# Optimization experiments

Measured on AMD Instinct MI355X. Metric: run time of the kernel, lower is better.

The kernel has to match this reference:

```python
import jax, jax.numpy as jnp
import numpy as np

EPS = 1e-6
NUM_HEADS = 16
ROPE_THETA = 100000.0


def _rope_tables(seq_len, head_dim, theta):
    inv_freq = 1.0 / (theta ** (np.arange(0, head_dim, 2, dtype=np.float32) / head_dim))
    t = np.arange(seq_len, dtype=np.float32)
    freqs = np.outer(t, inv_freq)                      # (S, head_dim//2)
    emb = np.concatenate([freqs, freqs], axis=-1)      # (S, head_dim)
    return jnp.asarray(np.cos(emb))[None], jnp.asarray(np.sin(emb))[None]  # (1,S,D)


def setup_inputs() -> dict:
    key = jax.random.key(0)
    ks = jax.random.split(key, 6)
    B, S, H = 2, 2048, 1024
    head_dim = H // NUM_HEADS
    cos, sin = _rope_tables(S, head_dim, ROPE_THETA)
    scale = 0.02
    return {
        "hidden_states": jax.random.normal(ks[0], (B, S, H), dtype=jnp.float32),
        "cos": cos, "sin": sin,
        "Wq": jax.random.normal(ks[1], (H, H), dtype=jnp.float32) * scale,
        "bq": jnp.zeros((H,), dtype=jnp.float32),
        "Wk": jax.random.normal(ks[2], (H, H), dtype=jnp.float32) * scale,
        "bk": jnp.zeros((H,), dtype=jnp.float32),
        "Wv": jax.random.normal(ks[3], (H, H), dtype=jnp.float32) * scale,
        "bv": jnp.zeros((H,), dtype=jnp.float32),
        "Wo": jax.random.normal(ks[4], (H, H), dtype=jnp.float32) * scale,
        "bo": jnp.zeros((H,), dtype=jnp.float32),
        "rms_weight": jnp.ones((H,), dtype=jnp.float32),
    }


def _rms_norm(x, w):
    var = jnp.mean(x * x, axis=-1, keepdims=True)
    return x * jax.lax.rsqrt(var + EPS) * w


def _rotate_half(x):
    x1, x2 = jnp.split(x, 2, axis=-1)
    return jnp.concatenate([-x2, x1], axis=-1)


def reference(hidden_states, cos, sin, Wq, bq, Wk, bk, Wv, bv, Wo, bo, rms_weight):
    B, S, H = hidden_states.shape
    D = H // NUM_HEADS
    q = hidden_states @ Wq.T + bq
    k = hidden_states @ Wk.T + bk
    v = hidden_states @ Wv.T + bv
    # RMSNorm over full hidden dim BEFORE head split (as in original)
    q = _rms_norm(q, rms_weight)
    k = _rms_norm(k, rms_weight)
    # (B,S,H) -> (B,heads,S,D)
    q = q.reshape(B, S, NUM_HEADS, D).transpose(0, 2, 1, 3)
    k = k.reshape(B, S, NUM_HEADS, D).transpose(0, 2, 1, 3)
    v = v.reshape(B, S, NUM_HEADS, D).transpose(0, 2, 1, 3)
    # RoPE: cos/sin (1,S,D) -> unsqueeze head dim
    c = cos[:, None, :, :]
    s = sin[:, None, :, :]
    q = q * c + _rotate_half(q) * s
    k = k * c + _rotate_half(k) * s
    # attention (faithful: boolean tril mask is ADDED as 0/1, not -inf)
    scale = D ** 0.5
    scores = jnp.einsum("bhqd,bhkd->bhqk", q, k) / scale
    mask = jnp.tril(jnp.ones((S, S), dtype=scores.dtype))  # +1 on causal, +0 elsewhere
    attn = jax.nn.softmax(scores + mask, axis=-1)
    out = jnp.einsum("bhqk,bhkd->bhqd", attn, v)
    out = out.transpose(0, 2, 1, 3).reshape(B, S, H)
    return out @ Wo.T + bo
```

## Files before the change

### kernel.cpp

```cpp
#include <hip/hip_runtime.h>

typedef unsigned short u16;
typedef __attribute__((ext_vector_type(8))) _Float16 half8;
typedef __attribute__((ext_vector_type(2))) __fp16 fp16x2;
typedef __attribute__((ext_vector_type(4))) float f32x4;
typedef __attribute__((ext_vector_type(16))) float f32x16;

#define MFMAH(A,B,C) __builtin_amdgcn_mfma_f32_16x16x32_f16(A,B,C,0,0,0)
#define MFMA32(A,B,C) __builtin_amdgcn_mfma_f32_32x32x16_f16(A,B,C,0,0,0)
#define LOG2E 1.4426950408889634f
#define C1 0.18033688011112042f

__device__ __forceinline__ u16 f2h(float f){
  _Float16 h = (_Float16)f; u16 r; __builtin_memcpy(&r,&h,2); return r;
}
__device__ __forceinline__ float h2f(u16 v){
  _Float16 h; __builtin_memcpy(&h,&v,2); return (float)h;
}
__device__ __forceinline__ unsigned int pack_h2(float a, float b){
  fp16x2 h = __builtin_amdgcn_cvt_pkrtz(a,b);
  unsigned int r; __builtin_memcpy(&r,&h,4); return r;
}

__device__ __forceinline__ void async_ld16(const void* g, void* l) {
  __builtin_amdgcn_global_load_lds(
      (const __attribute__((address_space(1))) unsigned int*)g,
      (__attribute__((address_space(3))) unsigned int*)l, 16, 0, 0);
}

__global__ __launch_bounds__(256) void cast_all(const float* __restrict__ hs,
    const float* __restrict__ wq, const float* __restrict__ wk,
    const float* __restrict__ wv, const float* __restrict__ wo,
    u16* __restrict__ dst)
{
  unsigned int i = blockIdx.x*256 + threadIdx.x;
  size_t el = (size_t)i * 8;
  const float* src; size_t off;
  if (el < 4194304) { src = hs; off = el; }
  else {
    unsigned int r = (unsigned int)((el - 4194304) >> 20);
    src = (r==0)?wq:(r==1)?wk:(r==2)?wv:wo;
    off = (el - 4194304) & 1048575;
  }
  float4 a = *reinterpret_cast<const float4*>(src+off);
  float4 b = *reinterpret_cast<const float4*>(src+off+4);
  uint4 o = {pack_h2(a.x,a.y), pack_h2(a.z,a.w), pack_h2(b.x,b.y), pack_h2(b.z,b.w)};
  *reinterpret_cast<uint4*>(dst + el) = o;
}

__global__ __launch_bounds__(256) void gemm_qkv(const u16* __restrict__ A,
                                                const u16* __restrict__ W,
                                                const float* __restrict__ bqp,
                                                const float* __restrict__ bkp,
                                                const float* __restrict__ bvp,
                                                u16* __restrict__ qout,
                                                u16* __restrict__ kout,
                                                u16* __restrict__ vout,
                                                int M, int K)
{
  __shared__ __align__(16) u16 lds_a[128*32];
  __shared__ __align__(16) u16 lds_w[128*32];
  const int t = threadIdx.x;
  const int lane = t & 63, wave = t >> 6;
  const int wm = wave >> 1, wn = wave & 1;
  const int lr = lane & 15, quad = lane >> 4;
  const int n0 = blockIdx.x * 128, m0 = blockIdx.y * 128;
  const int wbase = t & 192;
  const int which = n0 >> 10;

  const f32x4 fzero = {0.f,0.f,0.f,0.f};
  f32x4 acc[4][4];
  #pragma unroll
  for (int i=0;i<4;++i)
    #pragma unroll
    for (int j=0;j<4;++j) acc[i][j] = fzero;

  if (which < 2) {
    for (int k0 = 0; k0 < K; k0 += 32) {
      __syncthreads();
      #pragma unroll
      for (int it=0; it<2; ++it) {
        int idx = it*256 + t;
        int row = idx >> 2, c8 = (idx & 3) * 8;
        int lbase = (it*256 + wbase) * 8;
        async_ld16(&A[(size_t)(m0+row)*K + k0 + c8], &lds_a[lbase]);
        async_ld16(&W[(size_t)(n0+row)*K + k0 + c8], &lds_w[lbase]);
      }
      __syncthreads();
      half8 af[4], bfr[4];
      #pragma unroll
      for (int mt=0; mt<4; ++mt)
        af[mt] = *reinterpret_cast<const half8*>(&lds_a[(wm*64 + mt*16 + lr)*32 + quad*8]);
      #pragma unroll
      for (int nt=0; nt<4; ++nt)
        bfr[nt] = *reinterpret_cast<const half8*>(&lds_w[(wn*64 + nt*16 + lr)*32 + quad*8]);
      #pragma unroll
      for (int mt=0; mt<4; ++mt)
        #pragma unroll
        for (int nt=0; nt<4; ++nt)
          acc[mt][nt] = MFMAH(bfr[nt], af[mt], acc[mt][nt]);
    }
    const float* bp = which ? bkp : bqp;
    u16* dst = which ? kout : qout;
    #pragma unroll
    for (int nt=0; nt<4; ++nt) {
      int nn = (n0 & 1023) + wn*64 + nt*16 + quad*4;
      float4 bv = *reinterpret_cast<const float4*>(&bp[nn]);
      int hh = nn >> 6, d4 = nn & 63;
      #pragma unroll
      for (int mt=0; mt<4; ++mt) {
        int m = m0 + wm*64 + mt*16 + lr;
        int b = m >> 11, s = m & 2047;
        uint2 o = {pack_h2(acc[mt][nt][0]+bv.x, acc[mt][nt][1]+bv.y),
                   pack_h2(acc[mt][nt][2]+bv.z, acc[mt][nt][3]+bv.w)};
        *reinterpret_cast<uint2*>(&dst[((size_t)(b*16 + hh)*2048 + s)*64 + d4]) = o;
      }
    }
  } else {
    for (int k0 = 0; k0 < K; k0 += 32) {
      __syncthreads();
      #pragma unroll
      for (int it=0; it<2; ++it) {
        int idx = it*256 + t;
        int row = idx >> 2, c8 = (idx & 3) * 8;
        int lbase = (it*256 + wbase) * 8;
        async_ld16(&A[(size_t)(m0+row)*K + k0 + c8], &lds_a[lbase]);
        async_ld16(&W[(size_t)(n0+row)*K + k0 + c8], &lds_w[lbase]);
      }
      __syncthreads();
      half8 af[4], bfr[4];
      #pragma unroll
      for (int mt=0; mt<4; ++mt)
        af[mt] = *reinterpret_cast<const half8*>(&lds_a[(wm*64 + mt*16 + lr)*32 + quad*8]);
      #pragma unroll
      for (int nt=0; nt<4; ++nt)
        bfr[nt] = *reinterpret_cast<const half8*>(&lds_w[(wn*64 + nt*16 + lr)*32 + quad*8]);
      #pragma unroll
      for (int mt=0; mt<4; ++mt)
        #pragma unroll
        for (int nt=0; nt<4; ++nt)
          acc[mt][nt] = MFMAH(af[mt], bfr[nt], acc[mt][nt]);
    }
    #pragma unroll
    for (int nt=0; nt<4; ++nt) {
      int nn = (n0 & 1023) + wn*64 + nt*16 + lr;
      float bv = bvp[nn];
      int hh = nn >> 6, d = nn & 63;
      #pragma unroll
      for (int mt=0; mt<4; ++mt) {
        int m = m0 + wm*64 + mt*16 + quad*4;
        int b = m >> 11, s = m & 2047;
        uint2 o = {pack_h2(acc[mt][nt][0]+bv, acc[mt][nt][1]+bv),
                   pack_h2(acc[mt][nt][2]+bv, acc[mt][nt][3]+bv)};
        *reinterpret_cast<uint2*>(&vout[((size_t)(b*16 + hh)*64 + d)*2048 + s]) = o;
      }
    }
  }
}

__global__ __launch_bounds__(256) void gemm_o(const u16* __restrict__ A,
                                              const u16* __restrict__ W,
                                              const float* __restrict__ bias,
                                              float* __restrict__ O,
                                              int M, int N, int K)
{
  __shared__ __align__(16) u16 lds_a[128*32];
  __shared__ __align__(16) u16 lds_w[64*32];
  const int t = threadIdx.x;
  const int lane = t & 63, wm = t >> 6;
  const int lr = lane & 15, quad = lane >> 4;
  const int n0 = blockIdx.x * 64, m0 = blockIdx.y * 128;
  const int wbase = t & 192;

  const f32x4 fzero = {0.f,0.f,0.f,0.f};
  f32x4 acc[2][4];
  #pragma unroll
  for (int i=0;i<2;++i)
    #pragma unroll
    for (int j=0;j<4;++j) acc[i][j] = fzero;

  for (int k0 = 0; k0 < K; k0 += 32) {
    __syncthreads();
    #pragma unroll
    for (int it=0; it<2; ++it) {
      int idx = it*256 + t;
      int row = idx >> 2, c8 = (idx & 3) * 8;
      int lbase = (it*256 + wbase) * 8;
      async_ld16(&A[(size_t)(m0+row)*K + k0 + c8], &lds_a[lbase]);
    }
    async_ld16(&W[(size_t)(n0 + (t>>2))*K + k0 + (t&3)*8], &lds_w[wbase*8]);
    __syncthreads();
    half8 af[2], bfr[4];
    #pragma unroll
    for (int mt=0; mt<2; ++mt)
      af[mt] = *reinterpret_cast<const half8*>(&lds_a[(wm*32 + mt*16 + lr)*32 + quad*8]);
    #pragma unroll
    for (int nt=0; nt<4; ++nt)
      bfr[nt] = *reinterpret_cast<const half8*>(&lds_w[(nt*16 + lr)*32 + quad*8]);
    #pragma unroll
    for (int mt=0; mt<2; ++mt)
      #pragma unroll
      for (int nt=0; nt<4; ++nt)
        acc[mt][nt] = MFMAH(bfr[nt], af[mt], acc[mt][nt]);
  }

  #pragma unroll
  for (int nt=0; nt<4; ++nt) {
    int nb = n0 + nt*16 + quad*4;
    float4 bv = *reinterpret_cast<const float4*>(&bias[nb]);
    #pragma unroll
    for (int mt=0; mt<2; ++mt) {
      int m = m0 + wm*32 + mt*16 + lr;
      float4 o = {acc[mt][nt][0]+bv.x, acc[mt][nt][1]+bv.y,
                  acc[mt][nt][2]+bv.z, acc[mt][nt][3]+bv.w};
      *reinterpret_cast<float4*>(&O[(size_t)m * N + nb]) = o;
    }
  }
}

__global__ __launch_bounds__(128) void rmsrope(u16* __restrict__ qb, u16* __restrict__ kb,
                                               const float* __restrict__ cosb,
                                               const float* __restrict__ sinb,
                                               const float* __restrict__ w)
{
  u16* buf = blockIdx.y ? kb : qb;
  const int bs = blockIdx.x;
  const int b = bs >> 11, s = bs & 2047;
  const int t = threadIdx.x;
  const int h = t >> 3, d0 = (t & 7) * 4;
  size_t base = ((size_t)(b*16+h)*2048 + s)*64;

  uint2 u1 = *reinterpret_cast<const uint2*>(&buf[base + d0]);
  uint2 u2 = *reinterpret_cast<const uint2*>(&buf[base + d0 + 32]);
  u16 a1[4], a2[4];
  __builtin_memcpy(a1, &u1, 8); __builtin_memcpy(a2, &u2, 8);
  float x1[4], x2[4];
  float ss = 0.f;
  #pragma unroll
  for (int j=0;j<4;++j){
    x1[j] = h2f(a1[j]); x2[j] = h2f(a2[j]);
    ss += x1[j]*x1[j] + x2[j]*x2[j];
  }
  #pragma unroll
  for (int off=32; off>0; off>>=1) ss += __shfl_xor(ss, off, 64);
  __shared__ float red[2];
  if ((t & 63) == 0) red[t>>6] = ss;
  __syncthreads();
  float tot = red[0] + red[1];
  float r = rsqrtf(tot * (1.0f/1024.0f) + 1e-6f);

  float4 w1 = *reinterpret_cast<const float4*>(&w[h*64+d0]);
  float4 w2 = *reinterpret_cast<const float4*>(&w[h*64+d0+32]);
  float4 c1 = *reinterpret_cast<const float4*>(&cosb[s*64+d0]);
  float4 s1 = *reinterpret_cast<const float4*>(&sinb[s*64+d0]);
  float4 c2 = *reinterpret_cast<const float4*>(&cosb[s*64+d0+32]);
  float4 s2 = *reinterpret_cast<const float4*>(&sinb[s*64+d0+32]);
  float n1[4] = {x1[0]*r*w1.x, x1[1]*r*w1.y, x1[2]*r*w1.z, x1[3]*r*w1.w};
  float n2[4] = {x2[0]*r*w2.x, x2[1]*r*w2.y, x2[2]*r*w2.z, x2[3]*r*w2.w};
  float o1[4] = {n1[0]*c1.x - n2[0]*s1.x, n1[1]*c1.y - n2[1]*s1.y,
                 n1[2]*c1.z - n2[2]*s1.z, n1[3]*c1.w - n2[3]*s1.w};
  float o2[4] = {n2[0]*c2.x + n1[0]*s2.x, n2[1]*c2.y + n1[1]*s2.y,
                 n2[2]*c2.z + n1[2]*s2.z, n2[3]*c2.w + n1[3]*s2.w};
  uint2 v1 = {pack_h2(o1[0],o1[1]), pack_h2(o1[2],o1[3])};
  uint2 v2 = {pack_h2(o2[0],o2[1]), pack_h2(o2[2],o2[3])};
  *reinterpret_cast<uint2*>(&buf[base + d0])      = v1;
  *reinterpret_cast<uint2*>(&buf[base + d0 + 32]) = v2;
}

__global__ __launch_bounds__(256) void attn(const u16* __restrict__ qh,
                                            const u16* __restrict__ kh,
                                            const u16* __restrict__ vt,
                                            u16* __restrict__ ao)
{
  __shared__ __align__(16) u16 kbuf[2][64*72];
  __shared__ __align__(16) u16 vbuf[2][64*72];
  const int t = threadIdx.x;
  const int lane = t & 63, w = t >> 6;
  const int ql = lane & 31, hf = lane >> 5;
  const int qbase = blockIdx.x * 128;
  const int bh = blockIdx.y;
  const int b = bh >> 4, h = bh & 15;
  const size_t hb = (size_t)bh * 2048 * 64;
  const u16* qp = qh + hb;
  const u16* kp = kh + hb;
  const u16* vtp = vt + hb;

  const int q_abs = qbase + w*32 + ql;
  half8 qf[4];
  #pragma unroll
  for (int s=0;s<4;++s)
    qf[s] = *reinterpret_cast<const half8*>(&qp[(size_t)q_abs*64 + s*16 + hf*8]);

  const int row = t >> 3;
  const int cc = t & 7;
  const int base2 = 32*(cc>>2) + 16*((cc>>1)&1) + 4*(cc&1);
  const int kofs = row*72 + cc*8;
  const u16* kg = kp + (size_t)row*64 + cc*8;
  const u16* vg = vtp + (size_t)row*2048 + base2;

  const f32x16 fz16 = {0.f,0.f,0.f,0.f,0.f,0.f,0.f,0.f,0.f,0.f,0.f,0.f,0.f,0.f,0.f,0.f};
  f32x16 oacc[2];
  oacc[0] = fz16; oacc[1] = fz16;
  float lsum = 0.f;
  const int diag = (qbase + w*32) >> 6;

  {
    uint4 k0v = *reinterpret_cast<const uint4*>(kg);
    uint4 k1v = *reinterpret_cast<const uint4*>(kg + 32*64);
    uint2 a0 = *reinterpret_cast<const uint2*>(vg);
    uint2 a1 = *reinterpret_cast<const uint2*>(vg + 8);
    uint2 b0 = *reinterpret_cast<const uint2*>(vg + (size_t)32*2048);
    uint2 b1 = *reinterpret_cast<const uint2*>(vg + (size_t)32*2048 + 8);
    *reinterpret_cast<uint4*>(&kbuf[0][kofs])        = k0v;
    *reinterpret_cast<uint4*>(&kbuf[0][kofs+32*72])  = k1v;
    uint4 v0 = {a0.x,a0.y,a1.x,a1.y};
    uint4 v1 = {b0.x,b0.y,b1.x,b1.y};
    *reinterpret_cast<uint4*>(&vbuf[0][kofs])        = v0;
    *reinterpret_cast<uint4*>(&vbuf[0][kofs+32*72])  = v1;
  }

  for (int kt=0; kt<32; ++kt) {
    uint4 k0n, k1n; uint2 a0n, a1n, b0n, b1n;
    if (kt < 31) {
      const u16* kgn = kg + (size_t)(kt+1)*4096;
      const u16* vgn = vg + (kt+1)*64;
      k0n = *reinterpret_cast<const uint4*>(kgn);
      k1n = *reinterpret_cast<const uint4*>(kgn + 32*64);
      a0n = *reinterpret_cast<const uint2*>(vgn);
      a1n = *reinterpret_cast<const uint2*>(vgn + 8);
      b0n = *reinterpret_cast<const uint2*>(vgn + (size_t)32*2048);
      b1n = *reinterpret_cast<const uint2*>(vgn + (size_t)32*2048 + 8);
    }
    __syncthreads();
    const u16* kb = kbuf[kt & 1];
    const u16* vb = vbuf[kt & 1];

    unsigned int pk[4][4];
    #pragma unroll
    for (int kh2=0; kh2<2; ++kh2) {
      f32x16 z = fz16;
      #pragma unroll
      for (int s=0;s<4;++s) {
        half8 kf;
        __builtin_memcpy(&kf, &kb[(kh2*32+ql)*72 + s*16 + hf*8], 16);
        z = MFMA32(kf, qf[s], z);
      }
      float p[16];
      if (kt != diag) {
        float ml = (kt < diag) ? LOG2E : 0.0f;
        #pragma unroll
        for (int r=0;r<16;++r) {
          p[r] = __builtin_amdgcn_exp2f(__builtin_fmaf(z[r], C1, ml));
          lsum += p[r];
        }
      } else {
        #pragma unroll
        for (int r=0;r<16;++r) {
          int key = kt*64 + kh2*32 + (r&3) + 8*(r>>2) + 4*hf;
          float ml = (key <= q_abs) ? LOG2E : 0.0f;
          p[r] = __builtin_amdgcn_exp2f(__builtin_fmaf(z[r], C1, ml));
          lsum += p[r];
        }
      }
      #pragma unroll
      for (int t2=0;t2<2;++t2)
        #pragma unroll
        for (int jj=0;jj<4;++jj)
          pk[kh2*2+t2][jj] = pack_h2(p[t2*8+jj*2], p[t2*8+jj*2+1]);
    }

    #pragma unroll
    for (int st=0;st<4;++st) {
      uint4 pq = {pk[st][0], pk[st][1], pk[st][2], pk[st][3]};
      half8 pf; __builtin_memcpy(&pf, &pq, 16);
      #pragma unroll
      for (int dh=0; dh<2; ++dh) {
        half8 vf;
        __builtin_memcpy(&vf, &vb[(dh*32+ql)*72 + st*16 + hf*8], 16);
        oacc[dh] = MFMA32(vf, pf, oacc[dh]);
      }
    }

    if (kt < 31) {
      u16* kwn = &kbuf[(kt+1)&1][kofs];
      u16* vwn = &vbuf[(kt+1)&1][kofs];
      *reinterpret_cast<uint4*>(kwn)         = k0n;
      *reinterpret_cast<uint4*>(kwn + 32*72) = k1n;
      uint4 v0 = {a0n.x,a0n.y,a1n.x,a1n.y};
      uint4 v1 = {b0n.x,b0n.y,b1n.x,b1n.y};
      *reinterpret_cast<uint4*>(vwn)         = v0;
      *reinterpret_cast<uint4*>(vwn + 32*72) = v1;
    }
  }

  lsum += __shfl_xor(lsum, 32, 64);
  float inv = 1.0f / lsum;
  size_t rowbase = ((size_t)(b*2048 + q_abs))*1024 + h*64;
  #pragma unroll
  for (int dh=0; dh<2; ++dh)
    #pragma unroll
    for (int rq=0; rq<4; ++rq) {
      int dd = dh*32 + 8*rq + 4*hf;
      uint2 o = {pack_h2(oacc[dh][rq*4+0]*inv, oacc[dh][rq*4+1]*inv),
                 pack_h2(oacc[dh][rq*4+2]*inv, oacc[dh][rq*4+3]*inv)};
      *reinterpret_cast<uint2*>(&ao[rowbase + dd]) = o;
    }
}

extern "C" void kernel_launch(void* const* d_in, const int* in_sizes, int n_in,
                              void* d_out, int out_size, void* d_ws, size_t ws_size,
                              hipStream_t stream)
{
  const float* hs   = (const float*)d_in[0];
  const float* cosb = (const float*)d_in[1];
  const float* sinb = (const float*)d_in[2];
  const float* Wq   = (const float*)d_in[3];
  const float* bq   = (const float*)d_in[4];
  const float* Wk   = (const float*)d_in[5];
  const float* bk   = (const float*)d_in[6];
  const float* Wv   = (const float*)d_in[7];
  const float* bv   = (const float*)d_in[8];
  const float* Wo   = (const float*)d_in[9];
  const float* bo   = (const float*)d_in[10];
  const float* rw   = (const float*)d_in[11];

  const size_t NEL = (size_t)4096 * 1024;
  const size_t WEL = (size_t)1024 * 1024;
  u16* hsb = (u16*)d_ws;
  u16* wqb = hsb + NEL;
  u16* wob = wqb + 3*WEL;
  u16* qhb = wob + WEL;
  u16* khb = qhb + NEL;
  u16* vtb = khb + NEL;
  u16* aob = hsb;

  cast_all<<<4096, 256, 0, stream>>>(hs, Wq, Wk, Wv, Wo, hsb);
  gemm_qkv<<<dim3(24,32), 256, 0, stream>>>(hsb, wqb, bq, bk, bv, qhb, khb, vtb, 4096, 1024);
  rmsrope<<<dim3(4096,2), 128, 0, stream>>>(qhb, khb, cosb, sinb, rw);
  attn<<<dim3(16,32), 256, 0, stream>>>(qhb, khb, vtb, aob);
  gemm_o<<<dim3(16,32), 256, 0, stream>>>(aob, wob, bo, (float*)d_out, 4096, 1024, 1024);
}
```

Before: 220.1 us.

## Split attention KV loop across two wave groups with LDS reduction

Doubles the attention block to 512 threads, with two groups of four waves each handling alternate 64-key tiles for the same 128 queries. Each group keeps its own double-buffered K/V in shared memory, and at the end group 1 writes its partial output and row sums to LDS for group 0 to add and normalize. This halves the serial KV loop per wave and raises occupancy on the 512-block grid. The cost is twice the LDS per block, an extra reduction pass through shared memory, and fewer resident blocks per CU.

```diff
diff --git a/kernel.cpp b/kernel.cpp
--- a/kernel.cpp
+++ b/kernel.cpp
@@ -267,15 +267,15 @@
   *reinterpret_cast<uint2*>(&buf[base + d0 + 32]) = v2;
 }
 
-__global__ __launch_bounds__(256) void attn(const u16* __restrict__ qh,
+__global__ __launch_bounds__(512) void attn(const u16* __restrict__ qh,
                                             const u16* __restrict__ kh,
                                             const u16* __restrict__ vt,
                                             u16* __restrict__ ao)
 {
-  __shared__ __align__(16) u16 kbuf[2][64*72];
-  __shared__ __align__(16) u16 vbuf[2][64*72];
+  __shared__ __align__(16) u16 kvb[2][2][2][64*72];
   const int t = threadIdx.x;
   const int lane = t & 63, w = t >> 6;
+  const int g = w >> 2, wl = w & 3;
   const int ql = lane & 31, hf = lane >> 5;
   const int qbase = blockIdx.x * 128;
   const int bh = blockIdx.y;
@@ -285,14 +285,15 @@
   const u16* kp = kh + hb;
   const u16* vtp = vt + hb;
 
-  const int q_abs = qbase + w*32 + ql;
+  const int q_abs = qbase + wl*32 + ql;
   half8 qf[4];
   #pragma unroll
   for (int s=0;s<4;++s)
     qf[s] = *reinterpret_cast<const half8*>(&qp[(size_t)q_abs*64 + s*16 + hf*8]);
 
-  const int row = t >> 3;
-  const int cc = t & 7;
+  const int tl = t & 255;
+  const int row = tl >> 3;
+  const int cc = tl & 7;
   const int base2 = 32*(cc>>2) + 16*((cc>>1)&1) + 4*(cc&1);
   const int kofs = row*72 + cc*8;
   const u16* kg = kp + (size_t)row*64 + cc*8;
@@ -302,28 +303,31 @@
   f32x16 oacc[2];
   oacc[0] = fz16; oacc[1] = fz16;
   float lsum = 0.f;
-  const int diag = (qbase + w*32) >> 6;
+  const int diag = (qbase + wl*32) >> 6;
 
   {
-    uint4 k0v = *reinterpret_cast<const uint4*>(kg);
-    uint4 k1v = *reinterpret_cast<const uint4*>(kg + 32*64);
-    uint2 a0 = *reinterpret_cast<const uint2*>(vg);
-    uint2 a1 = *reinterpret_cast<const uint2*>(vg + 8);
-    uint2 b0 = *reinterpret_cast<const uint2*>(vg + (size_t)32*2048);
-    uint2 b1 = *reinterpret_cast<const uint2*>(vg + (size_t)32*2048 + 8);
-    *reinterpret_cast<uint4*>(&kbuf[0][kofs])        = k0v;
-    *reinterpret_cast<uint4*>(&kbuf[0][kofs+32*72])  = k1v;
+    const u16* kgs = kg + (size_t)g*4096;
+    const u16* vgs = vg + g*64;
+    uint4 k0v = *reinterpret_cast<const uint4*>(kgs);
+    uint4 k1v = *reinterpret_cast<const uint4*>(kgs + 32*64);
+    uint2 a0 = *reinterpret_cast<const uint2*>(vgs);
+    uint2 a1 = *reinterpret_cast<const uint2*>(vgs + 8);
+    uint2 b0 = *reinterpret_cast<const uint2*>(vgs + (size_t)32*2048);
+    uint2 b1 = *reinterpret_cast<const uint2*>(vgs + (size_t)32*2048 + 8);
+    *reinterpret_cast<uint4*>(&kvb[g][0][0][kofs])        = k0v;
+    *reinterpret_cast<uint4*>(&kvb[g][0][0][kofs+32*72])  = k1v;
     uint4 v0 = {a0.x,a0.y,a1.x,a1.y};
     uint4 v1 = {b0.x,b0.y,b1.x,b1.y};
-    *reinterpret_cast<uint4*>(&vbuf[0][kofs])        = v0;
-    *reinterpret_cast<uint4*>(&vbuf[0][kofs+32*72])  = v1;
-  }
-
-  for (int kt=0; kt<32; ++kt) {
+    *reinterpret_cast<uint4*>(&kvb[g][1][0][kofs])        = v0;
+    *reinterpret_cast<uint4*>(&kvb[g][1][0][kofs+32*72])  = v1;
+  }
+
+  for (int i=0; i<16; ++i) {
+    const int kt = 2*i + g;
     uint4 k0n, k1n; uint2 a0n, a1n, b0n, b1n;
-    if (kt < 31) {
-      const u16* kgn = kg + (size_t)(kt+1)*4096;
-      const u16* vgn = vg + (kt+1)*64;
+    if (i < 15) {
+      const u16* kgn = kg + (size_t)(kt+2)*4096;
+      const u16* vgn = vg + (kt+2)*64;
       k0n = *reinterpret_cast<const uint4*>(kgn);
       k1n = *reinterpret_cast<const uint4*>(kgn + 32*64);
       a0n = *reinterpret_cast<const uint2*>(vgn);
@@ -332,8 +336,8 @@
       b1n = *reinterpret_cast<const uint2*>(vgn + (size_t)32*2048 + 8);
     }
     __syncthreads();
-    const u16* kb = kbuf[kt & 1];
-    const u16* vb = vbuf[kt & 1];
+    const u16* kb = kvb[g][0][i&1];
+    const u16* vb = kvb[g][1][i&1];
 
     unsigned int pk[4][4];
     #pragma unroll
@@ -381,9 +385,9 @@
       }
     }
 
-    if (kt < 31) {
-      u16* kwn = &kbuf[(kt+1)&1][kofs];
-      u16* vwn = &vbuf[(kt+1)&1][kofs];
+    if (i < 15) {
+      u16* kwn = &kvb[g][0][(i+1)&1][kofs];
+      u16* vwn = &kvb[g][1][(i+1)&1][kofs];
       *reinterpret_cast<uint4*>(kwn)         = k0n;
       *reinterpret_cast<uint4*>(kwn + 32*72) = k1n;
       uint4 v0 = {a0n.x,a0n.y,a1n.x,a1n.y};
@@ -393,18 +397,38 @@
     }
   }
 
-  lsum += __shfl_xor(lsum, 32, 64);
-  float inv = 1.0f / lsum;
-  size_t rowbase = ((size_t)(b*2048 + q_abs))*1024 + h*64;
-  #pragma unroll
-  for (int dh=0; dh<2; ++dh)
-    #pragma unroll
-    for (int rq=0; rq<4; ++rq) {
-      int dd = dh*32 + 8*rq + 4*hf;
-      uint2 o = {pack_h2(oacc[dh][rq*4+0]*inv, oacc[dh][rq*4+1]*inv),
-                 pack_h2(oacc[dh][rq*4+2]*inv, oacc[dh][rq*4+3]*inv)};
-      *reinterpret_cast<uint2*>(&ao[rowbase + dd]) = o;
-    }
+  __syncthreads();
+  float* comb = reinterpret_cast<float*>(&kvb[1][0][0][0]);
+  const int slot = wl*64 + lane;
+  if (g == 1) {
+    #pragma unroll
+    for (int dh=0; dh<2; ++dh)
+      #pragma unroll
+      for (int r=0; r<16; ++r)
+        comb[(dh*16+r)*256 + slot] = oacc[dh][r];
+    comb[32*256 + slot] = lsum;
+  }
+  __syncthreads();
+  if (g == 0) {
+    #pragma unroll
+    for (int dh=0; dh<2; ++dh)
+      #pragma unroll
+      for (int r=0; r<16; ++r)
+        oacc[dh][r] += comb[(dh*16+r)*256 + slot];
+    lsum += comb[32*256 + slot];
+    lsum += __shfl_xor(lsum, 32, 64);
+    float inv = 1.0f / lsum;
+    size_t rowbase = ((size_t)(b*2048 + q_abs))*1024 + h*64;
+    #pragma unroll
+    for (int dh=0; dh<2; ++dh)
+      #pragma unroll
+      for (int rq=0; rq<4; ++rq) {
+        int dd = dh*32 + 8*rq + 4*hf;
+        uint2 o = {pack_h2(oacc[dh][rq*4+0]*inv, oacc[dh][rq*4+1]*inv),
+                   pack_h2(oacc[dh][rq*4+2]*inv, oacc[dh][rq*4+3]*inv)};
+        *reinterpret_cast<uint2*>(&ao[rowbase + dd]) = o;
+      }
+  }
 }
 
 extern "C" void kernel_launch(void* const* d_in, const int* in_sizes, int n_in,
@@ -437,6 +461,6 @@
   cast_all<<<4096, 256, 0, stream>>>(hs, Wq, Wk, Wv, Wo, hsb);
   gemm_qkv<<<dim3(24,32), 256, 0, stream>>>(hsb, wqb, bq, bk, bv, qhb, khb, vtb, 4096, 1024);
   rmsrope<<<dim3(4096,2), 128, 0, stream>>>(qhb, khb, cosb, sinb, rw);
-  attn<<<dim3(16,32), 256, 0, stream>>>(qhb, khb, vtb, aob);
+  attn<<<dim3(16,32), 512, 0, stream>>>(qhb, khb, vtb, aob);
   gemm_o<<<dim3(16,32), 256, 0, stream>>>(aob, wob, bo, (float*)d_out, 4096, 1024, 1024);
 }
```

Result: slower. 225.5 us (+2.4%).
